# Performance work log

Measured on AMD Instinct MI355X. Metric: run time of the kernel, lower is better.

## Reference

```python
import jax, jax.numpy as jnp
import numpy as np

RANK = 16
ALPHA = 16.0
IN_F = 4096
OUT_F = 11008
TOKENS = 64


def setup_inputs() -> dict:
    key = jax.random.key(0)
    k_x, k_w, k_s, k_a, k_b, k_bias = jax.random.split(key, 6)
    return {
        "x": jax.random.normal(k_x, (TOKENS, IN_F), dtype=jnp.float32),
        "weight_int4": jax.random.normal(k_w, (OUT_F, IN_F), dtype=jnp.float32),
        "weight_scale": jax.random.uniform(k_s, (OUT_F,), dtype=jnp.float32),
        "lora_A": jax.random.normal(k_a, (RANK, IN_F), dtype=jnp.float32) * 0.01,
        "lora_B": jax.random.normal(k_b, (OUT_F, RANK), dtype=jnp.float32),
        "bias": jax.random.normal(k_bias, (OUT_F,), dtype=jnp.float32),
    }


def reference(x, weight_int4, weight_scale, lora_A, lora_B, bias):
    # Dequantize: per-output-channel scale.  [out, in]
    weight = weight_int4 * weight_scale[:, None]
    # LoRA delta: B @ A scaled by alpha/rank.  [out, in]
    lora_weight = (lora_B @ lora_A) * (ALPHA / RANK)
    effective_weight = weight + lora_weight
    # F.linear: x @ W^T + b  ->  [tokens, out]
    return x @ effective_weight.T + bias
```

## Files before the change

### kernel.cpp

```cpp
#include <hip/hip_runtime.h>
#include <hip/hip_bf16.h>
#include <cstdint>

#define TOK   64
#define INF   4096
#define OUTF  11008
#define KCHUNKS 128
#define QCNT  8
#define NCHB  172

using bf16x8  = __attribute__((ext_vector_type(8))) __bf16;
using floatx4 = __attribute__((ext_vector_type(4))) float;

union B8u { uint32_t u[4]; uint4 q; bf16x8 v; };

__device__ __forceinline__ uint32_t hi2(float a, float b) {
    return (__float_as_uint(a) >> 16) | (__float_as_uint(b) & 0xffff0000u);
}
__device__ __forceinline__ float losub(float x) {
    return x - __uint_as_float(__float_as_uint(x) & 0xffff0000u);
}
__device__ __forceinline__ void packW(float4 a, float4 b, B8u& wh, B8u& wl) {
    wh.u[0] = hi2(a.x, a.y);  wh.u[1] = hi2(a.z, a.w);
    wh.u[2] = hi2(b.x, b.y);  wh.u[3] = hi2(b.z, b.w);
    wl.u[0] = hi2(losub(a.x), losub(a.y));
    wl.u[1] = hi2(losub(a.z), losub(a.w));
    wl.u[2] = hi2(losub(b.x), losub(b.y));
    wl.u[3] = hi2(losub(b.z), losub(b.w));
}

__global__ __launch_bounds__(256) void k_prep_x(const float* __restrict__ x,
        unsigned short* __restrict__ xh, unsigned short* __restrict__ xl) {
    int idx  = blockIdx.x * 256 + threadIdx.x;
    int j    = idx & 7;
    int lane = (idx >> 3) & 63;
    int kc   = (idx >> 9) & 127;
    int mt   = idx >> 16;
    int row  = mt * 16 + (lane & 15);
    int col  = kc * 32 + ((lane >> 4) << 3) + j;
    float v  = x[(size_t)row * INF + col];
    uint32_t u = __float_as_uint(v);
    float lo = losub(v);
    xh[idx] = (unsigned short)(u >> 16);
    xl[idx] = (unsigned short)(__float_as_uint(lo) >> 16);
}

__global__ __launch_bounds__(256) void k_lora_t(const float* __restrict__ x,
        const float* __restrict__ A, float* __restrict__ tm) {
    int t = blockIdx.x, wv = threadIdx.x >> 6, lane = threadIdx.x & 63;
    int r = blockIdx.y * 4 + wv;
    const float4* xr = (const float4*)(x + (size_t)t * INF);
    const float4* ar = (const float4*)(A + (size_t)r * INF);
    float s = 0.f;
#pragma unroll
    for (int i = 0; i < INF / 4 / 64; ++i) {
        float4 a = xr[lane + i * 64], b = ar[lane + i * 64];
        s += a.x * b.x + a.y * b.y + a.z * b.z + a.w * b.w;
    }
#pragma unroll
    for (int off = 32; off > 0; off >>= 1) s += __shfl_down(s, off);
    if (lane == 0) tm[t * 16 + r] = s;
}

template<bool ATOMIC>
__global__ __launch_bounds__(256, 2) void k_main(const float* __restrict__ W,
        const uint4* __restrict__ xh, const uint4* __restrict__ xl,
        const float* __restrict__ scale, float* __restrict__ part,
        float* __restrict__ out) {
    __shared__ uint4 wlds[2048];
    __shared__ uint4 xsl[2048];

    int tid  = threadIdx.x;
    int lane = tid & 63;
    int wv   = tid >> 6;
    int quad = lane >> 4;
    int nb   = blockIdx.x % NCHB;
    int q    = blockIdx.x / NCHB;
    int chl  = wv * 16 + (lane & 15);
    int ch   = nb * 64 + chl;

    const int kbase = q * 512;
    int rpar = lane >> 5;
    int gg   = lane & 31;

    floatx4 acc[4] = {};

    for (int ph = 0; ph < 4; ++ph) {
        __syncthreads();

#pragma unroll
        for (int t = 0; t < 8; ++t) {
            int i = wv * 8 + t;
            int r = i * 2 + rpar;
            int f = (gg - r) & 31;
            const float* src = W + (size_t)(nb * 64 + r) * INF
                             + kbase + ph * 128 + f * 4;
            __builtin_amdgcn_global_load_lds(
                (const __attribute__((address_space(1))) uint32_t*)src,
                (__attribute__((address_space(3))) uint32_t*)&wlds[i * 64],
                16, 0, 0);
        }
#pragma unroll
        for (int t = 0; t < 8; ++t) {
            int j  = wv * 8 + t;
            int hl = j >> 4, mt = (j >> 2) & 3, kc = j & 3;
            const uint4* src = (hl ? xl : xh)
                + ((size_t)(mt * KCHUNKS + q * 16 + ph * 4 + kc) * 64 + lane);
            __builtin_amdgcn_global_load_lds(
                (const __attribute__((address_space(1))) uint32_t*)src,
                (__attribute__((address_space(3))) uint32_t*)&xsl[j * 64],
                16, 0, 0);
        }
        __syncthreads();

#pragma unroll
        for (int kc = 0; kc < 4; ++kc) {
            int f0 = (kc * 4 + quad) * 2;
            uint4 wf0 = wlds[chl * 32 + ((f0 + chl) & 31)];
            uint4 wf1 = wlds[chl * 32 + ((f0 + 1 + chl) & 31)];
            B8u wh, wl;
            packW(*(float4*)&wf0, *(float4*)&wf1, wh, wl);
#pragma unroll
            for (int mt = 0; mt < 4; ++mt) {
                B8u ah, al;
                ah.q = xsl[(mt * 4 + kc) * 64 + lane];
                al.q = xsl[(16 + mt * 4 + kc) * 64 + lane];
                acc[mt] = __builtin_amdgcn_mfma_f32_16x16x32_bf16(ah.v, wh.v, acc[mt], 0, 0, 0);
                acc[mt] = __builtin_amdgcn_mfma_f32_16x16x32_bf16(ah.v, wl.v, acc[mt], 0, 0, 0);
                acc[mt] = __builtin_amdgcn_mfma_f32_16x16x32_bf16(al.v, wh.v, acc[mt], 0, 0, 0);
            }
        }
    }

#pragma unroll
    for (int mt = 0; mt < 4; ++mt) {
        int token = mt * 16 + quad * 4;
#pragma unroll
        for (int r = 0; r < 4; ++r) {
            if constexpr (ATOMIC) {
                atomicAdd(&out[(size_t)(token + r) * OUTF + ch], scale[ch] * acc[mt][r]);
            } else {
                part[((size_t)q * TOK + token + r) * OUTF + ch] = acc[mt][r];
            }
        }
    }
}

__global__ __launch_bounds__(256) void k_post(const float* __restrict__ part,
        const float* __restrict__ scale, const float* __restrict__ bias,
        const float* __restrict__ lB, const float* __restrict__ tm,
        float* __restrict__ out) {
    int o = blockIdx.x * 256 + threadIdx.x;
    int t = blockIdx.y;
    if (o >= OUTF) return;
    float s = 0.f;
#pragma unroll
    for (int qq = 0; qq < QCNT; ++qq)
        s += part[((size_t)qq * TOK + t) * OUTF + o];
    const float4* Br = (const float4*)(lB + (size_t)o * 16);
    const float4* tr = (const float4*)(tm + (size_t)t * 16);
    float l = 0.f;
#pragma unroll
    for (int i = 0; i < 4; ++i) {
        float4 b = Br[i], tt = tr[i];
        l += b.x * tt.x + b.y * tt.y + b.z * tt.z + b.w * tt.w;
    }
    out[(size_t)t * OUTF + o] = s * scale[o] + l + bias[o];
}

__global__ __launch_bounds__(256) void k_pre(const float* __restrict__ bias,
        const float* __restrict__ lB, const float* __restrict__ tm,
        float* __restrict__ out) {
    int o = blockIdx.x * 256 + threadIdx.x;
    int t = blockIdx.y;
    if (o >= OUTF) return;
    const float4* Br = (const float4*)(lB + (size_t)o * 16);
    const float4* tr = (const float4*)(tm + (size_t)t * 16);
    float l = 0.f;
#pragma unroll
    for (int i = 0; i < 4; ++i) {
        float4 b = Br[i], tt = tr[i];
        l += b.x * tt.x + b.y * tt.y + b.z * tt.z + b.w * tt.w;
    }
    out[(size_t)t * OUTF + o] = l + bias[o];
}

extern "C" void kernel_launch(void* const* d_in, const int* in_sizes, int n_in,
                              void* d_out, int out_size, void* d_ws, size_t ws_size,
                              hipStream_t stream) {
    const float* x     = (const float*)d_in[0];
    const float* W     = (const float*)d_in[1];
    const float* scale = (const float*)d_in[2];
    const float* lA    = (const float*)d_in[3];
    const float* lB    = (const float*)d_in[4];
    const float* bias  = (const float*)d_in[5];
    float* out = (float*)d_out;

    char* ws = (char*)d_ws;
    unsigned short* xh = (unsigned short*)(ws);
    unsigned short* xl = (unsigned short*)(ws + 524288);
    float* tm   = (float*)(ws + 1048576);
    float* part = (float*)(ws + 1052672);
    const size_t need = 1052672 + (size_t)QCNT * TOK * OUTF * 4;

    k_prep_x<<<1024, 256, 0, stream>>>(x, xh, xl);
    k_lora_t<<<dim3(TOK, 4), 256, 0, stream>>>(x, lA, tm);

    if (ws_size >= need) {
        k_main<false><<<NCHB * QCNT, 256, 0, stream>>>(W, (const uint4*)xh,
                (const uint4*)xl, scale, part, out);
        k_post<<<dim3(43, TOK), 256, 0, stream>>>(part, scale, bias, lB, tm, out);
    } else {
        k_pre<<<dim3(43, TOK), 256, 0, stream>>>(bias, lB, tm, out);
        k_main<true><<<NCHB * QCNT, 256, 0, stream>>>(W, (const uint4*)xh,
                (const uint4*)xl, scale, nullptr, out);
    }
}
```

Measured before the change: 272.8 us.

## Pipeline per-wave W loads through an LDS ring with vmcnt waits and double split-K

Measured after the change: 299.2 us. +9.7%, slower.

```diff
diff --git a/kernel.cpp b/kernel.cpp
--- a/kernel.cpp
+++ b/kernel.cpp
@@ -6,8 +6,9 @@
 #define INF   4096
 #define OUTF  11008
 #define KCHUNKS 128
-#define QCNT  8
+#define QCNT  16
 #define NCHB  172
+#define KC    8
 
 using bf16x8  = __attribute__((ext_vector_type(8))) __bf16;
 using floatx4 = __attribute__((ext_vector_type(4))) float;
@@ -27,6 +28,10 @@
     wl.u[1] = hi2(losub(a.z), losub(a.w));
     wl.u[2] = hi2(losub(b.x), losub(b.y));
     wl.u[3] = hi2(losub(b.z), losub(b.w));
+}
+
+template<int N> __device__ __forceinline__ void vmwait() {
+    asm volatile("s_waitcnt vmcnt(%0)" :: "n"(N) : "memory");
 }
 
 __global__ __launch_bounds__(256) void k_prep_x(const float* __restrict__ x,
@@ -63,75 +68,90 @@
 }
 
 template<bool ATOMIC>
-__global__ __launch_bounds__(256, 2) void k_main(const float* __restrict__ W,
+__global__ __launch_bounds__(256, 1) void k_main(const float* __restrict__ W,
         const uint4* __restrict__ xh, const uint4* __restrict__ xl,
         const float* __restrict__ scale, float* __restrict__ part,
         float* __restrict__ out) {
-    __shared__ uint4 wlds[2048];
-    __shared__ uint4 xsl[2048];
-
-    int tid  = threadIdx.x;
-    int lane = tid & 63;
-    int wv   = tid >> 6;
-    int quad = lane >> 4;
-    int nb   = blockIdx.x % NCHB;
-    int q    = blockIdx.x / NCHB;
-    int chl  = wv * 16 + (lane & 15);
-    int ch   = nb * 64 + chl;
-
-    const int kbase = q * 512;
-    int rpar = lane >> 5;
-    int gg   = lane & 31;
-
-    floatx4 acc[4] = {};
-
-    for (int ph = 0; ph < 4; ++ph) {
-        __syncthreads();
-
-#pragma unroll
-        for (int t = 0; t < 8; ++t) {
-            int i = wv * 8 + t;
-            int r = i * 2 + rpar;
-            int f = (gg - r) & 31;
-            const float* src = W + (size_t)(nb * 64 + r) * INF
-                             + kbase + ph * 128 + f * 4;
+    __shared__ uint4 xsl[2][4][KC][64];
+    __shared__ uint4 wring[4][4][128];
+
+    const int tid  = threadIdx.x;
+    const int lane = tid & 63;
+    const int wv   = tid >> 6;
+    const int quad = lane >> 4;
+    const int rr   = lane & 15;
+    const int nb   = blockIdx.x % NCHB;
+    const int q    = blockIdx.x / NCHB;
+
+    const int subrow = (lane >> 3) & 7;
+    const int gglob  = (lane & 7) ^ subrow;
+    const float* Wq  = W + (size_t)(nb * 64 + wv * 16) * INF + q * (KC * 32);
+
+#pragma unroll
+    for (int t = 0; t < 16; ++t) {
+        int j  = wv * 16 + t;
+        int hl = j >> 5, mt = (j >> 3) & 3, kc = j & 7;
+        const uint4* src = (hl ? xl : xh)
+            + ((size_t)(mt * KCHUNKS + q * KC + kc) * 64 + lane);
+        __builtin_amdgcn_global_load_lds(
+            (const __attribute__((address_space(1))) uint32_t*)src,
+            (__attribute__((address_space(3))) uint32_t*)&xsl[hl][mt][kc][0],
+            16, 0, 0);
+    }
+#pragma unroll
+    for (int s = 0; s < 3; ++s) {
+#pragma unroll
+        for (int i = 0; i < 2; ++i) {
+            const float* src = Wq + (size_t)(i * 8 + subrow) * INF + s * 32 + gglob * 4;
             __builtin_amdgcn_global_load_lds(
                 (const __attribute__((address_space(1))) uint32_t*)src,
-                (__attribute__((address_space(3))) uint32_t*)&wlds[i * 64],
+                (__attribute__((address_space(3))) uint32_t*)&wring[wv][s][i * 64],
                 16, 0, 0);
         }
-#pragma unroll
-        for (int t = 0; t < 8; ++t) {
-            int j  = wv * 8 + t;
-            int hl = j >> 4, mt = (j >> 2) & 3, kc = j & 3;
-            const uint4* src = (hl ? xl : xh)
-                + ((size_t)(mt * KCHUNKS + q * 16 + ph * 4 + kc) * 64 + lane);
-            __builtin_amdgcn_global_load_lds(
-                (const __attribute__((address_space(1))) uint32_t*)src,
-                (__attribute__((address_space(3))) uint32_t*)&xsl[j * 64],
-                16, 0, 0);
-        }
-        __syncthreads();
-
-#pragma unroll
-        for (int kc = 0; kc < 4; ++kc) {
-            int f0 = (kc * 4 + quad) * 2;
-            uint4 wf0 = wlds[chl * 32 + ((f0 + chl) & 31)];
-            uint4 wf1 = wlds[chl * 32 + ((f0 + 1 + chl) & 31)];
-            B8u wh, wl;
-            packW(*(float4*)&wf0, *(float4*)&wf1, wh, wl);
-#pragma unroll
-            for (int mt = 0; mt < 4; ++mt) {
-                B8u ah, al;
-                ah.q = xsl[(mt * 4 + kc) * 64 + lane];
-                al.q = xsl[(16 + mt * 4 + kc) * 64 + lane];
-                acc[mt] = __builtin_amdgcn_mfma_f32_16x16x32_bf16(ah.v, wh.v, acc[mt], 0, 0, 0);
-                acc[mt] = __builtin_amdgcn_mfma_f32_16x16x32_bf16(ah.v, wl.v, acc[mt], 0, 0, 0);
-                acc[mt] = __builtin_amdgcn_mfma_f32_16x16x32_bf16(al.v, wh.v, acc[mt], 0, 0, 0);
+    }
+    __syncthreads();
+
+    floatx4 acc[4] = {};
+
+#pragma unroll
+    for (int kc = 0; kc < KC; ++kc) {
+        if (kc + 3 < KC) {
+            int s = (kc + 3) & 3;
+#pragma unroll
+            for (int i = 0; i < 2; ++i) {
+                const float* src = Wq + (size_t)(i * 8 + subrow) * INF
+                                 + (kc + 3) * 32 + gglob * 4;
+                __builtin_amdgcn_global_load_lds(
+                    (const __attribute__((address_space(1))) uint32_t*)src,
+                    (__attribute__((address_space(3))) uint32_t*)&wring[wv][s][i * 64],
+                    16, 0, 0);
             }
         }
-    }
-
+        {
+            int lft = KC - 1 - kc;
+            int wc  = (lft > 3 ? 3 : lft) * 2;
+            if (wc == 6) vmwait<6>();
+            else if (wc == 4) vmwait<4>();
+            else if (wc == 2) vmwait<2>();
+            else vmwait<0>();
+        }
+        const uint4* slot = &wring[wv][kc & 3][0];
+        uint4 wf0 = slot[rr * 8 + ((quad * 2)     ^ (rr & 7))];
+        uint4 wf1 = slot[rr * 8 + ((quad * 2 + 1) ^ (rr & 7))];
+        B8u wh, wl;
+        packW(*(const float4*)&wf0, *(const float4*)&wf1, wh, wl);
+#pragma unroll
+        for (int mt = 0; mt < 4; ++mt) {
+            B8u ah, al;
+            ah.q = xsl[0][mt][kc][lane];
+            al.q = xsl[1][mt][kc][lane];
+            acc[mt] = __builtin_amdgcn_mfma_f32_16x16x32_bf16(ah.v, wh.v, acc[mt], 0, 0, 0);
+            acc[mt] = __builtin_amdgcn_mfma_f32_16x16x32_bf16(ah.v, wl.v, acc[mt], 0, 0, 0);
+            acc[mt] = __builtin_amdgcn_mfma_f32_16x16x32_bf16(al.v, wh.v, acc[mt], 0, 0, 0);
+        }
+    }
+
+    int ch = nb * 64 + wv * 16 + rr;
 #pragma unroll
     for (int mt = 0; mt < 4; ++mt) {
         int token = mt * 16 + quad * 4;
```
